# Kernel optimization log

Measured on AMD Instinct MI355X. Metric: run time of the kernel, lower is better.

The kernel has to match this reference:

```python
import jax, jax.numpy as jnp
import numpy as np

D_MODEL = 128; D_STATE = 8; D_CONV = 4; D_INNER = 256; DT_RANK = 8
H1 = 32; INPUTS = 3; OUTPUTS = 5
B_SZ = 8; SEQ = 2048


def _mamba(u, in_proj_w, conv_w, conv_b, x_proj_w, dt_proj_w, dt_proj_b, A_log, Dp, out_proj_w):
    # u: [B, L, D_MODEL]
    B, L, _ = u.shape
    xz = u @ in_proj_w.T                      # [B, L, 2*D_INNER]
    xs, z = jnp.split(xz, 2, axis=-1)
    # depthwise causal conv1d over time
    xc = jnp.moveaxis(xs, 1, 2)               # [B, D_INNER, L]
    xc = jax.lax.conv_general_dilated(
        xc, conv_w, window_strides=(1,), padding=[(D_CONV - 1, 0)],
        feature_group_count=D_INNER, dimension_numbers=("NCH", "OIH", "NCH"))
    xc = xc + conv_b[None, :, None]
    xs = jax.nn.silu(jnp.moveaxis(xc, 1, 2))  # [B, L, D_INNER]
    x_dbl = xs @ x_proj_w.T                   # [B, L, DT_RANK + 2*D_STATE]
    dt = x_dbl[..., :DT_RANK]
    Bm = x_dbl[..., DT_RANK:DT_RANK + D_STATE]
    Cm = x_dbl[..., DT_RANK + D_STATE:]
    delta = jax.nn.softplus(dt @ dt_proj_w.T + dt_proj_b)   # [B, L, D_INNER]
    A = -jnp.exp(A_log)                                     # [D_INNER, D_STATE]
    dA = jnp.exp(jnp.einsum("bld,dn->bldn", delta, A))      # [B, L, D_INNER, D_STATE]
    dBu = jnp.einsum("bld,bln->bldn", delta * xs, Bm)       # delta * B * u

    def step(h, t):
        dA_t, dBu_t, C_t = t
        h = dA_t * h + dBu_t                  # [B, D_INNER, D_STATE]
        y = jnp.einsum("bdn,bn->bd", h, C_t)
        return h, y

    h0 = jnp.zeros((B, D_INNER, D_STATE), dA.dtype)
    _, ys = jax.lax.scan(step, h0, (jnp.moveaxis(dA, 1, 0), jnp.moveaxis(dBu, 1, 0), jnp.moveaxis(Cm, 1, 0)))
    y = jnp.moveaxis(ys, 0, 1) + Dp * xs      # [B, L, D_INNER]
    y = y * jax.nn.silu(z)
    return y @ out_proj_w.T                   # [B, L, D_MODEL]


def _forward(x, proj0_w, proj0_b, in_proj_w, conv_w, conv_b, x_proj_w, dt_proj_w, dt_proj_b,
             A_log, Dp, out_proj_w, mlin_w, mlin_b, proj1_w, proj1_b, lin1_w, lin1_b,
             proj2_w, proj2_b):
    out = x @ proj0_w.T + proj0_b                            # proj0
    out = jnp.tanh(out)                                      # Dropout(1e-4) -> eval identity; Tanh
    out = _mamba(out, in_proj_w, conv_w, conv_b, x_proj_w, dt_proj_w, dt_proj_b, A_log, Dp, out_proj_w)
    out = jax.nn.elu(out)
    mamba_out = out @ mlin_w.T + mlin_b                      # Linear(128,128)
    out = mamba_out @ proj1_w.T + proj1_b                    # proj1
    out = jax.nn.elu(out)
    out = out @ lin1_w.T + lin1_b                            # linear_seq
    combined = jnp.concatenate([x, mamba_out, out], axis=-1) # dstack -> [B, L, 3+128+32]
    o = combined @ proj2_w.T + proj2_b                       # [B, L, 5]
    PI = np.float32(np.pi)
    for _ in range(2):                                       # special_rounding_operation x2
        o = o + jnp.sin(o * PI) * 0.5
    o = (o + 1.0) * 0.5
    o = o.at[:, :, 2:].add(1.0)
    real = jnp.stack([
        x[:, :, 0] + o[:, :, 0],
        x[:, :, 1] + x[:, :, 2] * (o[:, :, 1] / o[:, :, 2]),
        x[:, :, 2] * (o[:, :, 3] / o[:, :, 4]),
    ], axis=-1)
    return real


def setup_inputs() -> dict:
    key = jax.random.key(0)
    ks = jax.random.split(key, 12)
    def w(k, shape, s=0.05):
        return (jax.random.normal(k, shape) * s).astype(jnp.float32)
    A_init = jnp.log(jnp.tile(jnp.arange(1, D_STATE + 1, dtype=jnp.float32), (D_INNER, 1)))
    return {
        "x": jax.random.normal(ks[0], (B_SZ, SEQ, INPUTS), dtype=jnp.float32),
        "proj0_w": w(ks[1], (D_MODEL, INPUTS)), "proj0_b": jnp.zeros((D_MODEL,), jnp.float32),
        "in_proj_w": w(ks[2], (2 * D_INNER, D_MODEL)),
        "conv_w": w(ks[3], (D_INNER, 1, D_CONV)), "conv_b": jnp.zeros((D_INNER,), jnp.float32),
        "x_proj_w": w(ks[4], (DT_RANK + 2 * D_STATE, D_INNER)),
        "dt_proj_w": w(ks[5], (D_INNER, DT_RANK)),
        "dt_proj_b": jnp.full((D_INNER,), -4.6, jnp.float32),
        "A_log": A_init, "Dp": jnp.ones((D_INNER,), jnp.float32),
        "out_proj_w": w(ks[6], (D_MODEL, D_INNER)),
        "mlin_w": w(ks[7], (D_MODEL, D_MODEL)), "mlin_b": jnp.zeros((D_MODEL,), jnp.float32),
        "proj1_w": w(ks[8], (H1, D_MODEL)), "proj1_b": jnp.zeros((H1,), jnp.float32),
        "lin1_w": w(ks[9], (H1, H1)), "lin1_b": jnp.zeros((H1,), jnp.float32),
        "proj2_w": w(ks[10], (OUTPUTS, INPUTS + D_MODEL + H1)),
        "proj2_b": jnp.zeros((OUTPUTS,), jnp.float32),
    }


def reference(x, proj0_w, proj0_b, in_proj_w, conv_w, conv_b, x_proj_w, dt_proj_w, dt_proj_b,
              A_log, Dp, out_proj_w, mlin_w, mlin_b, proj1_w, proj1_b, lin1_w, lin1_b,
              proj2_w, proj2_b):
    return _forward(x, proj0_w, proj0_b, in_proj_w, conv_w, conv_b, x_proj_w, dt_proj_w,
                    dt_proj_b, A_log, Dp, out_proj_w, mlin_w, mlin_b, proj1_w, proj1_b,
                    lin1_w, lin1_b, proj2_w, proj2_b)
```

## Files before the change

### kernel.cpp

```cpp
#include <hip/hip_runtime.h>
#include <hip/hip_bf16.h>
#include <math.h>

#define TOKENS 16384
#define SEQLEN 2048
#define NCHUNK 64
#define LCHUNK 32
#define LOG2E 1.4426950408889634f

typedef __attribute__((ext_vector_type(8))) short bf16x8;
typedef __attribute__((ext_vector_type(8))) unsigned short u16x8;
typedef __attribute__((ext_vector_type(4))) float f32x4;

__device__ inline unsigned short f2bf(float f) {
    unsigned u = __float_as_uint(f);
    return (unsigned short)((u + 0x7FFF + ((u >> 16) & 1)) >> 16);
}
__device__ inline float bf2f(unsigned short b) {
    return __uint_as_float((unsigned)b << 16);
}
__device__ inline f32x4 mfma16(bf16x8 a, bf16x8 b, f32x4 c) {
    return __builtin_amdgcn_mfma_f32_16x16x32_bf16(a, b, c, 0, 0, 0);
}
__device__ inline float exp2_hw(float x) {
    float r; asm("v_exp_f32 %0, %1" : "=v"(r) : "v"(x)); return r;
}
__device__ inline float rcp_hw(float x) {
    float r; asm("v_rcp_f32 %0, %1" : "=v"(r) : "v"(x)); return r;
}
__device__ inline float fast_tanh(float x) {
    float ax = fabsf(x);
    float e = exp2_hw(2.885390081777927f * ax);
    float r = 1.f - 2.f*rcp_hw(e + 1.f);
    return copysignf(r, x);
}
__device__ inline float silu_hw(float v) {
    float e = exp2_hw(-LOG2E * v);
    return v * rcp_hw(1.f + e);
}

__global__ void k_prep2(const float* __restrict__ ipw, const float* __restrict__ opw,
                        const float* __restrict__ mlw,
                        const float* __restrict__ xpw, const float* __restrict__ dtw,
                        __hip_bfloat16* __restrict__ wi, __hip_bfloat16* __restrict__ wo,
                        __hip_bfloat16* __restrict__ wm, __hip_bfloat16* __restrict__ Wx) {
    int i = blockIdx.x * 256 + threadIdx.x;
    if (i < 65536) {
        int e = i;
        int chunk = e >> 9, ln = (e >> 3) & 63, j = e & 7;
        int g = chunk >> 4, kk = (chunk >> 2) & 3, w = chunk & 3;
        int r = ln & 15, q = ln >> 4;
        int row = g*64 + w*16 + r, col = kk*32 + q*8 + j;
        wi[i] = __float2bfloat16(ipw[row*128 + col]);
    } else if (i < 98304) {
        int e = i - 65536;
        int chunk = e >> 9, ln = (e >> 3) & 63, j = e & 7;
        int h = chunk >> 5, kk = (chunk >> 2) & 7, w = chunk & 3;
        int r = ln & 15, q = ln >> 4;
        int row = h*64 + w*16 + r, col = kk*32 + q*8 + j;
        wo[e] = __float2bfloat16(opw[row*256 + col]);
    } else if (i < 114688) {
        int e = i - 98304;
        int chunk = e >> 9, ln = (e >> 3) & 63, j = e & 7;
        int h = chunk >> 4, kk = (chunk >> 2) & 3, w = chunk & 3;
        int r = ln & 15, q = ln >> 4;
        int row = h*64 + w*16 + r, col = kk*32 + q*8 + j;
        wm[e] = __float2bfloat16(mlw[row*128 + col]);
    } else if (i < 196608) {
        int e = i - 114688;
        int chunk = e >> 9, ln = (e >> 3) & 63, j = e & 7;
        int g = chunk >> 5, kk = (chunk >> 2) & 7, w = chunk & 3;
        int r = ln & 15, q = ln >> 4;
        int n = g*64 + w*16 + r, k = kk*32 + q*8 + j;
        float v = 0.f;
        if (n < 256) {
            #pragma unroll
            for (int jj = 0; jj < 8; ++jj) v = fmaf(dtw[n*8+jj], xpw[jj*256+k], v);
        } else if (n < 272) {
            v = xpw[(n-248)*256 + k];
        }
        Wx[e] = __float2bfloat16(v);
    }
}

__global__ __launch_bounds__(256) void k_front(
    const float* __restrict__ x, const float* __restrict__ p0w,
    const float* __restrict__ p0b,
    const __hip_bfloat16* __restrict__ Wi,
    const __hip_bfloat16* __restrict__ Wx,
    const float* __restrict__ cw, const float* __restrict__ cb,
    const float* __restrict__ dpb, const float* __restrict__ A_log,
    __hip_bfloat16* __restrict__ zb,
    __hip_bfloat16* __restrict__ xsb,
    __hip_bfloat16* __restrict__ dlt,
    float* __restrict__ Bmo, float* __restrict__ Cmo,
    float* __restrict__ Ssum, unsigned short* __restrict__ Hend)
{
    __shared__ __align__(16) char smem[17408 + 17920];
    __shared__ float sx[48][3];
    __hip_bfloat16* U   = (__hip_bfloat16*)smem;
    __hip_bfloat16* AXS = (__hip_bfloat16*)smem;
    __hip_bfloat16* XCL = (__hip_bfloat16*)(smem + 17408);
    __hip_bfloat16* DL  = (__hip_bfloat16*)(smem + 17408);
    float* SB           = (float*)(smem + 17408 + 16896);

    int tid = threadIdx.x;
    int blk = blockIdx.x;
    int tok0 = blk * 32;
    bool seqstart = (tok0 & (SEQLEN-1)) == 0;

    if (tid < 144) {
        int row = tid/3, c = tid%3;
        int tok = tok0 - 16 + row;
        if (tok < 0) tok = 0;
        sx[row][c] = x[(size_t)tok*3 + c];
    }
    __syncthreads();
    {
        int col = tid & 127;
        int r0 = tid >> 7;
        float w0 = p0w[col*3+0], w1 = p0w[col*3+1], w2 = p0w[col*3+2];
        float b  = p0b[col];
        #pragma unroll
        for (int it = 0; it < 24; ++it) {
            int row = r0 + it*2;
            float v = b + sx[row][0]*w0 + sx[row][1]*w1 + sx[row][2]*w2;
            U[row*144 + col] = __float2bfloat16(fast_tanh(v));
        }
    }
    __syncthreads();

    int ln = tid & 63, w = tid >> 6;
    int r = ln & 15, q = ln >> 4;
    int ln8 = ln * 8;

    {
        f32x4 acch[4];
        #pragma unroll
        for (int g = 0; g < 4; ++g) acch[g] = (f32x4){0.f,0.f,0.f,0.f};
        const __hip_bfloat16* ah = &U[r*144 + q*8];
        #pragma unroll
        for (int kk = 0; kk < 4; ++kk) {
            bf16x8 a = *(const bf16x8*)(ah + kk*32);
            #pragma unroll
            for (int g = 0; g < 4; ++g) {
                bf16x8 bfv = *(const bf16x8*)(Wi + (((g*4 + kk)*4 + w) << 9) + ln8);
                acch[g] = mfma16(a, bfv, acch[g]);
            }
        }
        #pragma unroll
        for (int g = 0; g < 4; ++g) {
            int col = g*64 + w*16 + r;
            #pragma unroll
            for (int rr = 0; rr < 4; ++rr) {
                int row = q*4 + rr;
                if (row >= 13) {
                    int j = row - 13;
                    XCL[j*256 + col] = seqstart ? __float2bfloat16(0.f)
                                                : __float2bfloat16(acch[g][rr]);
                }
            }
        }
    }
    {
        f32x4 acc[2][8];
        #pragma unroll
        for (int mi = 0; mi < 2; ++mi)
            #pragma unroll
            for (int g = 0; g < 8; ++g) acc[mi][g] = (f32x4){0.f,0.f,0.f,0.f};
        const __hip_bfloat16* a0p = &U[(16+r)*144 + q*8];
        const __hip_bfloat16* a1p = &U[(32+r)*144 + q*8];
        #pragma unroll
        for (int kk = 0; kk < 4; ++kk) {
            bf16x8 a0 = *(const bf16x8*)(a0p + kk*32);
            bf16x8 a1 = *(const bf16x8*)(a1p + kk*32);
            #pragma unroll
            for (int g = 0; g < 8; ++g) {
                bf16x8 bfv = *(const bf16x8*)(Wi + (((g*4 + kk)*4 + w) << 9) + ln8);
                acc[0][g] = mfma16(a0, bfv, acc[0][g]);
                acc[1][g] = mfma16(a1, bfv, acc[1][g]);
            }
        }
        #pragma unroll
        for (int g = 0; g < 8; ++g) {
            int col = g*64 + w*16 + r;
            #pragma unroll
            for (int mi = 0; mi < 2; ++mi) {
                #pragma unroll
                for (int rr = 0; rr < 4; ++rr) {
                    int m = mi*16 + q*4 + rr;
                    float v = acc[mi][g][rr];
                    if (col < 256) XCL[(m+3)*256 + col] = __float2bfloat16(v);
                    else zb[(size_t)(tok0+m)*256 + col - 256] = __float2bfloat16(v);
                }
            }
        }
    }
    __syncthreads();

    {
        int d = tid;
        float cw0 = cw[d*4+0], cw1 = cw[d*4+1], cw2 = cw[d*4+2], cw3 = cw[d*4+3];
        float cbd = cb[d];
        const unsigned short* xc0 = (const unsigned short*)XCL + d;
        float w0v = bf2f(xc0[0]);
        float w1v = bf2f(xc0[256]);
        float w2v = bf2f(xc0[512]);
        #pragma unroll
        for (int row = 0; row < 32; ++row) {
            float w3v = bf2f(xc0[(row+3)*256]);
            float acc = cbd;
            acc = fmaf(cw0, w0v, acc);
            acc = fmaf(cw1, w1v, acc);
            acc = fmaf(cw2, w2v, acc);
            acc = fmaf(cw3, w3v, acc);
            acc = silu_hw(acc);
            __hip_bfloat16 hv = __float2bfloat16(acc);
            AXS[row*272 + d] = hv;
            xsb[(size_t)(tok0 + row)*256 + d] = hv;
            w0v = w1v; w1v = w2v; w2v = w3v;
        }
    }
    __syncthreads();

    {
        f32x4 acc[2][5];
        #pragma unroll
        for (int mi = 0; mi < 2; ++mi)
            #pragma unroll
            for (int g = 0; g < 5; ++g) acc[mi][g] = (f32x4){0.f,0.f,0.f,0.f};
        const __hip_bfloat16* arow0 = &AXS[r*272 + q*8];
        const __hip_bfloat16* arow1 = &AXS[(16+r)*272 + q*8];
        #pragma unroll
        for (int kk = 0; kk < 8; ++kk) {
            bf16x8 a0 = *(const bf16x8*)(arow0 + kk*32);
            bf16x8 a1 = *(const bf16x8*)(arow1 + kk*32);
            #pragma unroll
            for (int g = 0; g < 5; ++g) {
                bf16x8 bfv = *(const bf16x8*)(Wx + (((g*8 + kk)*4 + w) << 9) + ln8);
                acc[0][g] = mfma16(a0, bfv, acc[0][g]);
                acc[1][g] = mfma16(a1, bfv, acc[1][g]);
            }
        }
        #pragma unroll
        for (int g = 0; g < 5; ++g) {
            int col = g*64 + w*16 + r;
            if (col >= 272) continue;
            #pragma unroll
            for (int mi = 0; mi < 2; ++mi) {
                #pragma unroll
                for (int rr = 0; rr < 4; ++rr) {
                    int t = mi*16 + q*4 + rr;
                    int row = tok0 + t;
                    float v = acc[mi][g][rr];
                    if (col < 256) {
                        v += dpb[col];
                        v = (v > 20.f) ? v : __logf(1.f + __expf(v));
                        __hip_bfloat16 hv = __float2bfloat16(v);
                        DL[t*264 + col] = hv;
                        dlt[(size_t)row*256 + col] = hv;
                    } else if (col < 264) {
                        SB[t*8 + col - 256] = v;
                        Bmo[(size_t)row*8 + col - 256] = v;
                    } else {
                        Cmo[(size_t)row*8 + col - 264] = v;
                    }
                }
            }
        }
    }
    __syncthreads();

    {
        int d = tid;
        float A2[8];
        #pragma unroll
        for (int n = 0; n < 8; ++n) A2[n] = -__expf(A_log[d*8+n]) * LOG2E;
        float h[8] = {};
        float S = 0.f;
        for (int t = 0; t < LCHUNK; ++t) {
            float dt_c = bf2f(*(const unsigned short*)&DL[t*264 + d]);
            float xt_c = bf2f(*(const unsigned short*)&AXS[t*272 + d]);
            S += dt_c;
            float dx = dt_c * xt_c;
            #pragma unroll
            for (int n = 0; n < 8; ++n)
                h[n] = fmaf(exp2_hw(A2[n]*dt_c), h[n], dx * SB[t*8 + n]);
        }
        Ssum[(size_t)blk*256 + d] = S;
        u16x8 hp;
        #pragma unroll
        for (int n = 0; n < 8; ++n) hp[n] = f2bf(h[n]);
        *(u16x8*)&Hend[((size_t)blk*256 + d)*8] = hp;
    }
}

__global__ void k_scomb(const float* __restrict__ Ssum, const unsigned short* __restrict__ Hend,
                        const float* __restrict__ A_log, unsigned short* __restrict__ Hin) {
    int blk = blockIdx.x;
    int b = blk >> 3, dg = blk & 7;
    int d = dg*32 + (threadIdx.x >> 3);
    int n = threadIdx.x & 7;
    float A2 = -__expf(A_log[d*8+n]) * LOG2E;
    float h = 0.f;
    size_t i0 = (size_t)(b*NCHUNK)*256 + d;
    float S  = Ssum[i0];
    float He = bf2f(Hend[i0*8 + n]);
    for (int c = 0; c < NCHUNK; ++c) {
        size_t idx = (size_t)(b*NCHUNK + c)*256 + d;
        float Sn = 0.f, Hn = 0.f;
        if (c < NCHUNK-1) {
            size_t ix2 = idx + 256;
            Sn = Ssum[ix2];
            Hn = bf2f(Hend[ix2*8 + n]);
        }
        Hin[idx*8 + n] = f2bf(h);
        h = fmaf(exp2_hw(A2*S), h, He);
        S = Sn; He = Hn;
    }
}

__global__ __launch_bounds__(256) void k_s2_opml(
    const __hip_bfloat16* __restrict__ delta,
    const __hip_bfloat16* __restrict__ xs,
    const float* __restrict__ Bm, const float* __restrict__ Cm,
    const __hip_bfloat16* __restrict__ zb,
    const float* __restrict__ A_log, const float* __restrict__ Dp,
    const unsigned short* __restrict__ Hin,
    const __hip_bfloat16* __restrict__ Wo,
    const __hip_bfloat16* __restrict__ Wm,
    const float* __restrict__ mlb,
    __hip_bfloat16* __restrict__ mo)
{
    __shared__ __hip_bfloat16 Al[32][272];
    __shared__ __hip_bfloat16 opl[32][136];
    __shared__ float sB[LCHUNK][8], sC[LCHUNK][8];
    int tid = threadIdx.x;
    int blk = blockIdx.x;
    int tok0 = blk * 32;
    {
        int t2 = tid >> 3, j = tid & 7;
        sB[t2][j] = Bm[(size_t)(tok0 + t2)*8 + j];
        sC[t2][j] = Cm[(size_t)(tok0 + t2)*8 + j];
    }
    int d = tid;
    float A2[8], h[8];
    u16x8 hv = *(const u16x8*)&Hin[((size_t)blk*256 + d)*8];
    #pragma unroll
    for (int n = 0; n < 8; ++n) {
        A2[n] = -__expf(A_log[d*8+n]) * LOG2E;
        h[n] = bf2f(hv[n]);
    }
    float Dpd = Dp[d];
    __syncthreads();
    const __hip_bfloat16* dptr = delta + (size_t)tok0*256 + d;
    const __hip_bfloat16* xptr = xs    + (size_t)tok0*256 + d;
    const __hip_bfloat16* zptr = zb    + (size_t)tok0*256 + d;
    float dt_c = __bfloat162float(dptr[0]), xt_c = __bfloat162float(xptr[0]);
    for (int t = 0; t < LCHUNK; ++t) {
        float dt_n = 0.f, xt_n = 0.f;
        if (t < LCHUNK-1) {
            dt_n = __bfloat162float(dptr[(t+1)*256]);
            xt_n = __bfloat162float(xptr[(t+1)*256]);
        }
        float dx = dt_c * xt_c;
        float yv = 0.f;
        #pragma unroll
        for (int n = 0; n < 8; ++n) {
            h[n] = fmaf(exp2_hw(A2[n]*dt_c), h[n], dx * sB[t][n]);
            yv = fmaf(h[n], sC[t][n], yv);
        }
        yv = fmaf(Dpd, xt_c, yv);
        float z = __bfloat162float(zptr[t*256]);
        yv *= silu_hw(z) * (z != 0.f ? 1.f : 1.f);
        Al[t][d] = __float2bfloat16(yv);
        dt_c = dt_n; xt_c = xt_n;
    }
    __syncthreads();

    int ln = tid & 63, w = tid >> 6;
    int r = ln & 15, q = ln >> 4;
    int ln8 = ln * 8;
    int c0 = w*16 + r, c1 = c0 + 64;

    f32x4 a00 = (f32x4){0.f,0.f,0.f,0.f};
    f32x4 a01 = a00, a10 = a00, a11 = a00;
    const __hip_bfloat16* a0p = &Al[r][q*8];
    const __hip_bfloat16* a1p = &Al[16+r][q*8];
    #pragma unroll
    for (int kk = 0; kk < 8; ++kk) {
        bf16x8 af0 = *(const bf16x8*)(a0p + kk*32);
        bf16x8 af1 = *(const bf16x8*)(a1p + kk*32);
        bf16x8 bf0 = *(const bf16x8*)(Wo + (((0*8 + kk)*4 + w) << 9) + ln8);
        bf16x8 bf1 = *(const bf16x8*)(Wo + (((1*8 + kk)*4 + w) << 9) + ln8);
        a00 = mfma16(af0, bf0, a00);
        a10 = mfma16(af1, bf0, a10);
        a01 = mfma16(af0, bf1, a01);
        a11 = mfma16(af1, bf1, a11);
    }
    #pragma unroll
    for (int rr = 0; rr < 4; ++rr) {
        int row = q*4 + rr;
        float v;
        v = a00[rr]; v = v > 0.f ? v : (__expf(v)-1.f); opl[row][c0]    = __float2bfloat16(v);
        v = a01[rr]; v = v > 0.f ? v : (__expf(v)-1.f); opl[row][c1]    = __float2bfloat16(v);
        v = a10[rr]; v = v > 0.f ? v : (__expf(v)-1.f); opl[row+16][c0] = __float2bfloat16(v);
        v = a11[rr]; v = v > 0.f ? v : (__expf(v)-1.f); opl[row+16][c1] = __float2bfloat16(v);
    }
    __syncthreads();

    f32x4 m00 = (f32x4){0.f,0.f,0.f,0.f};
    f32x4 m01 = m00, m10 = m00, m11 = m00;
    const __hip_bfloat16* A0m = &opl[r][q*8];
    const __hip_bfloat16* A1m = &opl[16+r][q*8];
    #pragma unroll
    for (int kk = 0; kk < 4; ++kk) {
        bf16x8 af0 = *(const bf16x8*)(A0m + kk*32);
        bf16x8 af1 = *(const bf16x8*)(A1m + kk*32);
        bf16x8 bf0 = *(const bf16x8*)(Wm + (((0*4 + kk)*4 + w) << 9) + ln8);
        bf16x8 bf1 = *(const bf16x8*)(Wm + (((1*4 + kk)*4 + w) << 9) + ln8);
        m00 = mfma16(af0, bf0, m00);
        m10 = mfma16(af1, bf0, m10);
        m01 = mfma16(af0, bf1, m01);
        m11 = mfma16(af1, bf1, m11);
    }
    {
        float bl0 = mlb[c0], bl1 = mlb[c1];
        __hip_bfloat16* mob = mo + (size_t)tok0*128;
        #pragma unroll
        for (int rr = 0; rr < 4; ++rr) {
            int row = q*4 + rr;
            mob[row*128 + c0]      = __float2bfloat16(m00[rr] + bl0);
            mob[row*128 + c1]      = __float2bfloat16(m01[rr] + bl1);
            mob[(row+16)*128 + c0] = __float2bfloat16(m10[rr] + bl0);
            mob[(row+16)*128 + c1] = __float2bfloat16(m11[rr] + bl1);
        }
    }
}

__global__ __launch_bounds__(256) void k_tail(const float* __restrict__ x,
                       const unsigned short* __restrict__ mo,
                       const float* __restrict__ p1w, const float* __restrict__ p1b,
                       const float* __restrict__ l1w, const float* __restrict__ l1b,
                       const float* __restrict__ p2w, const float* __restrict__ p2b,
                       float* __restrict__ out) {
    __shared__ float s_mo[16][132];
    __shared__ float s_p1w[32][132];
    __shared__ float s_l1w[32][36];
    __shared__ float s_p2w[5][164];
    __shared__ float s_h1[16][36];
    __shared__ float s_o32[16][36];
    __shared__ float s_o[16][6];
    int tid = threadIdx.x;
    int tok0 = blockIdx.x * 16;
    for (int i = tid; i < 32*32; i += 256) {
        int r = i >> 5, c = (i & 31) * 4;
        *(float4*)&s_p1w[r][c] = *(const float4*)&p1w[r*128 + c];
    }
    for (int i = tid; i < 32*8; i += 256) {
        int r = i >> 3, c = (i & 7) * 4;
        *(float4*)&s_l1w[r][c] = *(const float4*)&l1w[r*32 + c];
    }
    for (int i = tid; i < 5*163; i += 256)
        s_p2w[i / 163][i % 163] = p2w[i];
    {
        int i = tid;
        int r = i >> 4, c = (i & 15) * 8;
        u16x8 v = *(const u16x8*)&mo[(size_t)(tok0 + r)*128 + c];
        #pragma unroll
        for (int e = 0; e < 8; ++e) s_mo[r][c+e] = bf2f(v[e]);
    }
    __syncthreads();
    {
        int j = tid & 31, tb = tid >> 5;
        float bj = p1b[j];
        #pragma unroll
        for (int p = 0; p < 2; ++p) {
            int tk = tb + p*8;
            float v = bj;
            #pragma unroll 8
            for (int k = 0; k < 128; k += 4) {
                float4 m4 = *(const float4*)&s_mo[tk][k];
                float4 w4 = *(const float4*)&s_p1w[j][k];
                v = fmaf(m4.x, w4.x, v); v = fmaf(m4.y, w4.y, v);
                v = fmaf(m4.z, w4.z, v); v = fmaf(m4.w, w4.w, v);
            }
            v = v > 0.f ? v : (__expf(v) - 1.f);
            s_h1[tk][j] = v;
        }
    }
    __syncthreads();
    {
        int j = tid & 31, tb = tid >> 5;
        float bj = l1b[j];
        #pragma unroll
        for (int p = 0; p < 2; ++p) {
            int tk = tb + p*8;
            float v = bj;
            #pragma unroll
            for (int k = 0; k < 32; k += 4) {
                float4 m4 = *(const float4*)&s_h1[tk][k];
                float4 w4 = *(const float4*)&s_l1w[j][k];
                v = fmaf(m4.x, w4.x, v); v = fmaf(m4.y, w4.y, v);
                v = fmaf(m4.z, w4.z, v); v = fmaf(m4.w, w4.w, v);
            }
            s_o32[tk][j] = v;
        }
    }
    __syncthreads();
    if (tid < 160) {
        int tk = tid / 10, rem = tid % 10;
        int j = rem >> 1, half = rem & 1;
        const float* wr = s_p2w[j];
        float v = 0.f;
        if (half == 0) {
            int tok = tok0 + tk;
            v = fmaf(x[tok*3+0], wr[0], v);
            v = fmaf(x[tok*3+1], wr[1], v);
            v = fmaf(x[tok*3+2], wr[2], v);
            #pragma unroll 8
            for (int k = 0; k < 64; ++k) v = fmaf(s_mo[tk][k], wr[3+k], v);
        } else {
            #pragma unroll 8
            for (int k = 64; k < 128; ++k) v = fmaf(s_mo[tk][k], wr[3+k], v);
            #pragma unroll 8
            for (int k = 0; k < 32; ++k)  v = fmaf(s_o32[tk][k], wr[131+k], v);
        }
        v += __shfl_xor(v, 1);
        if (half == 0) {
            v += p2b[j];
            const float PI = 3.14159265358979323846f;
            v = v + __sinf(v*PI)*0.5f;
            v = v + __sinf(v*PI)*0.5f;
            v = (v + 1.f)*0.5f;
            if (j >= 2) v += 1.f;
            s_o[tk][j] = v;
        }
    }
    __syncthreads();
    if (tid < 48) {
        int tk = tid / 3, ln = tid % 3;
        int tok = tok0 + tk;
        float x0 = x[tok*3+0], x1 = x[tok*3+1], x2 = x[tok*3+2];
        float r;
        if (ln == 0)      r = x0 + s_o[tk][0];
        else if (ln == 1) r = x1 + x2*(s_o[tk][1]/s_o[tk][2]);
        else              r = x2*(s_o[tk][3]/s_o[tk][4]);
        out[(size_t)tok*3 + ln] = r;
    }
}

extern "C" void kernel_launch(void* const* d_in, const int* in_sizes, int n_in,
                              void* d_out, int out_size, void* d_ws, size_t ws_size,
                              hipStream_t stream) {
    const float* x        = (const float*)d_in[0];
    const float* proj0_w  = (const float*)d_in[1];
    const float* proj0_b  = (const float*)d_in[2];
    const float* in_proj_w= (const float*)d_in[3];
    const float* conv_w   = (const float*)d_in[4];
    const float* conv_b   = (const float*)d_in[5];
    const float* x_proj_w = (const float*)d_in[6];
    const float* dt_proj_w= (const float*)d_in[7];
    const float* dt_proj_b= (const float*)d_in[8];
    const float* A_log    = (const float*)d_in[9];
    const float* Dp       = (const float*)d_in[10];
    const float* out_proj_w=(const float*)d_in[11];
    const float* mlin_w   = (const float*)d_in[12];
    const float* mlin_b   = (const float*)d_in[13];
    const float* proj1_w  = (const float*)d_in[14];
    const float* proj1_b  = (const float*)d_in[15];
    const float* lin1_w   = (const float*)d_in[16];
    const float* lin1_b   = (const float*)d_in[17];
    const float* proj2_w  = (const float*)d_in[18];
    const float* proj2_b  = (const float*)d_in[19];
    float* out = (float*)d_out;

    char* wsb = (char*)d_ws;
    const size_t MB = 1048576;
    __hip_bfloat16* z_bf   = (__hip_bfloat16*)(wsb + 12*MB);
    __hip_bfloat16* xs_bf  = (__hip_bfloat16*)(wsb + 20*MB);
    __hip_bfloat16* dlt_bf = (__hip_bfloat16*)(wsb + 28*MB);
    float* Bm   = (float*)(wsb + 36*MB);
    float* Cm   = (float*)(wsb + 36*MB + 524288);
    float* Ssum = (float*)(wsb + 37*MB);
    unsigned short* Hend = (unsigned short*)(wsb + 37*MB + 524288);
    unsigned short* Hin  = (unsigned short*)(wsb + 39*MB + 524288);
    __hip_bfloat16* w_in_bf  = (__hip_bfloat16*)(wsb + 50*MB);
    __hip_bfloat16* w_out_bf = (__hip_bfloat16*)(wsb + 50*MB + 131072);
    __hip_bfloat16* w_ml_bf  = (__hip_bfloat16*)(wsb + 50*MB + 196608);
    __hip_bfloat16* Wx_bf    = (__hip_bfloat16*)(wsb + 50*MB + 229376);
    unsigned short* mo = (unsigned short*)(wsb + 51*MB);

    k_prep2<<<768, 256, 0, stream>>>(in_proj_w, out_proj_w, mlin_w, x_proj_w,
                                     dt_proj_w, w_in_bf, w_out_bf, w_ml_bf, Wx_bf);
    k_front<<<TOKENS/32, 256, 0, stream>>>(x, proj0_w, proj0_b, w_in_bf, Wx_bf,
                                           conv_w, conv_b, dt_proj_b, A_log,
                                           z_bf, xs_bf, dlt_bf, Bm, Cm, Ssum, Hend);
    k_scomb<<<64, 256, 0, stream>>>(Ssum, Hend, A_log, Hin);
    k_s2_opml<<<TOKENS/32, 256, 0, stream>>>(dlt_bf, xs_bf, Bm, Cm, z_bf, A_log, Dp,
                                             Hin, w_out_bf, w_ml_bf, mlin_b,
                                             (__hip_bfloat16*)mo);
    k_tail<<<TOKENS/16, 256, 0, stream>>>(x, mo, proj1_w, proj1_b, lin1_w, lin1_b, proj2_w, proj2_b, out);
}
```

Measured before the change: 83.35 us.

## Fuse tail MLP into scan/out-proj kernel, keeping mlin output in LDS

The separate tail kernel is merged into the second scan/out-projection kernel. The mlin output now stays in shared memory as bf16-rounded floats instead of being written to global memory and read back, and one kernel launch is dropped. The cost is higher LDS use per block (the tail weights are staged into every block), which may lower occupancy in the scan-heavy kernel. It also adds weight-loading work to each of the 512 blocks.

Measured after the change: 77.55 us. -7.0%, faster.

```diff
diff --git a/kernel.cpp b/kernel.cpp
--- a/kernel.cpp
+++ b/kernel.cpp
@@ -98,11 +98,11 @@
 {
     __shared__ __align__(16) char smem[17408 + 17920];
     __shared__ float sx[48][3];
+    __shared__ float SB[LCHUNK][8];
     __hip_bfloat16* U   = (__hip_bfloat16*)smem;
     __hip_bfloat16* AXS = (__hip_bfloat16*)smem;
     __hip_bfloat16* XCL = (__hip_bfloat16*)(smem + 17408);
     __hip_bfloat16* DL  = (__hip_bfloat16*)(smem + 17408);
-    float* SB           = (float*)(smem + 17408 + 16896);
 
     int tid = threadIdx.x;
     int blk = blockIdx.x;
@@ -260,7 +260,7 @@
                         DL[t*264 + col] = hv;
                         dlt[(size_t)row*256 + col] = hv;
                     } else if (col < 264) {
-                        SB[t*8 + col - 256] = v;
+                        SB[t][col - 256] = v;
                         Bmo[(size_t)row*8 + col - 256] = v;
                     } else {
                         Cmo[(size_t)row*8 + col - 264] = v;
@@ -285,7 +285,7 @@
             float dx = dt_c * xt_c;
             #pragma unroll
             for (int n = 0; n < 8; ++n)
-                h[n] = fmaf(exp2_hw(A2[n]*dt_c), h[n], dx * SB[t*8 + n]);
+                h[n] = fmaf(exp2_hw(A2[n]*dt_c), h[n], dx * SB[t][n]);
         }
         Ssum[(size_t)blk*256 + d] = S;
         u16x8 hp;
@@ -320,7 +320,7 @@
     }
 }
 
-__global__ __launch_bounds__(256) void k_s2_opml(
+__global__ __launch_bounds__(256) void k_s2_tail(
     const __hip_bfloat16* __restrict__ delta,
     const __hip_bfloat16* __restrict__ xs,
     const float* __restrict__ Bm, const float* __restrict__ Cm,
@@ -330,11 +330,24 @@
     const __hip_bfloat16* __restrict__ Wo,
     const __hip_bfloat16* __restrict__ Wm,
     const float* __restrict__ mlb,
-    __hip_bfloat16* __restrict__ mo)
+    const float* __restrict__ x,
+    const float* __restrict__ p1w, const float* __restrict__ p1b,
+    const float* __restrict__ l1w, const float* __restrict__ l1b,
+    const float* __restrict__ p2w, const float* __restrict__ p2b,
+    float* __restrict__ out)
 {
-    __shared__ __hip_bfloat16 Al[32][272];
+    __shared__ __align__(16) char smA[17408];
     __shared__ __hip_bfloat16 opl[32][136];
     __shared__ float sB[LCHUNK][8], sC[LCHUNK][8];
+    __shared__ float s_p1w[32][132];
+    __shared__ float s_l1w[32][36];
+    __shared__ float s_p2w[5][164];
+    __shared__ float s_h1[32][36];
+    __shared__ float s_o32[32][36];
+    __shared__ float s_o[32][6];
+    __hip_bfloat16* Al = (__hip_bfloat16*)smA;
+    float* mol = (float*)smA;
+
     int tid = threadIdx.x;
     int blk = blockIdx.x;
     int tok0 = blk * 32;
@@ -343,6 +356,16 @@
         sB[t2][j] = Bm[(size_t)(tok0 + t2)*8 + j];
         sC[t2][j] = Cm[(size_t)(tok0 + t2)*8 + j];
     }
+    for (int i = tid; i < 32*32; i += 256) {
+        int r2 = i >> 5, c2 = (i & 31) * 4;
+        *(float4*)&s_p1w[r2][c2] = *(const float4*)&p1w[r2*128 + c2];
+    }
+    {
+        int r2 = tid >> 3, c2 = (tid & 7) * 4;
+        *(float4*)&s_l1w[r2][c2] = *(const float4*)&l1w[r2*32 + c2];
+    }
+    for (int i = tid; i < 5*163; i += 256) s_p2w[i/163][i%163] = p2w[i];
+
     int d = tid;
     float A2[8], h[8];
     u16x8 hv = *(const u16x8*)&Hin[((size_t)blk*256 + d)*8];
@@ -372,8 +395,8 @@
         }
         yv = fmaf(Dpd, xt_c, yv);
         float z = __bfloat162float(zptr[t*256]);
-        yv *= silu_hw(z) * (z != 0.f ? 1.f : 1.f);
-        Al[t][d] = __float2bfloat16(yv);
+        yv *= silu_hw(z);
+        Al[t*272 + d] = __float2bfloat16(yv);
         dt_c = dt_n; xt_c = xt_n;
     }
     __syncthreads();
@@ -385,8 +408,8 @@
 
     f32x4 a00 = (f32x4){0.f,0.f,0.f,0.f};
     f32x4 a01 = a00, a10 = a00, a11 = a00;
-    const __hip_bfloat16* a0p = &Al[r][q*8];
-    const __hip_bfloat16* a1p = &Al[16+r][q*8];
+    const __hip_bfloat16* a0p = &Al[r*272 + q*8];
+    const __hip_bfloat16* a1p = &Al[(16+r)*272 + q*8];
     #pragma unroll
     for (int kk = 0; kk < 8; ++kk) {
         bf16x8 af0 = *(const bf16x8*)(a0p + kk*32);
@@ -426,61 +449,27 @@
     }
     {
         float bl0 = mlb[c0], bl1 = mlb[c1];
-        __hip_bfloat16* mob = mo + (size_t)tok0*128;
         #pragma unroll
         for (int rr = 0; rr < 4; ++rr) {
             int row = q*4 + rr;
-            mob[row*128 + c0]      = __float2bfloat16(m00[rr] + bl0);
-            mob[row*128 + c1]      = __float2bfloat16(m01[rr] + bl1);
-            mob[(row+16)*128 + c0] = __float2bfloat16(m10[rr] + bl0);
-            mob[(row+16)*128 + c1] = __float2bfloat16(m11[rr] + bl1);
-        }
-    }
-}
-
-__global__ __launch_bounds__(256) void k_tail(const float* __restrict__ x,
-                       const unsigned short* __restrict__ mo,
-                       const float* __restrict__ p1w, const float* __restrict__ p1b,
-                       const float* __restrict__ l1w, const float* __restrict__ l1b,
-                       const float* __restrict__ p2w, const float* __restrict__ p2b,
-                       float* __restrict__ out) {
-    __shared__ float s_mo[16][132];
-    __shared__ float s_p1w[32][132];
-    __shared__ float s_l1w[32][36];
-    __shared__ float s_p2w[5][164];
-    __shared__ float s_h1[16][36];
-    __shared__ float s_o32[16][36];
-    __shared__ float s_o[16][6];
-    int tid = threadIdx.x;
-    int tok0 = blockIdx.x * 16;
-    for (int i = tid; i < 32*32; i += 256) {
-        int r = i >> 5, c = (i & 31) * 4;
-        *(float4*)&s_p1w[r][c] = *(const float4*)&p1w[r*128 + c];
-    }
-    for (int i = tid; i < 32*8; i += 256) {
-        int r = i >> 3, c = (i & 7) * 4;
-        *(float4*)&s_l1w[r][c] = *(const float4*)&l1w[r*32 + c];
-    }
-    for (int i = tid; i < 5*163; i += 256)
-        s_p2w[i / 163][i % 163] = p2w[i];
-    {
-        int i = tid;
-        int r = i >> 4, c = (i & 15) * 8;
-        u16x8 v = *(const u16x8*)&mo[(size_t)(tok0 + r)*128 + c];
-        #pragma unroll
-        for (int e = 0; e < 8; ++e) s_mo[r][c+e] = bf2f(v[e]);
-    }
-    __syncthreads();
+            mol[row*132 + c0]      = bf2f(f2bf(m00[rr] + bl0));
+            mol[row*132 + c1]      = bf2f(f2bf(m01[rr] + bl1));
+            mol[(row+16)*132 + c0] = bf2f(f2bf(m10[rr] + bl0));
+            mol[(row+16)*132 + c1] = bf2f(f2bf(m11[rr] + bl1));
+        }
+    }
+    __syncthreads();
+
     {
         int j = tid & 31, tb = tid >> 5;
         float bj = p1b[j];
         #pragma unroll
-        for (int p = 0; p < 2; ++p) {
+        for (int p = 0; p < 4; ++p) {
             int tk = tb + p*8;
             float v = bj;
             #pragma unroll 8
             for (int k = 0; k < 128; k += 4) {
-                float4 m4 = *(const float4*)&s_mo[tk][k];
+                float4 m4 = *(const float4*)&mol[tk*132 + k];
                 float4 w4 = *(const float4*)&s_p1w[j][k];
                 v = fmaf(m4.x, w4.x, v); v = fmaf(m4.y, w4.y, v);
                 v = fmaf(m4.z, w4.z, v); v = fmaf(m4.w, w4.w, v);
@@ -494,7 +483,7 @@
         int j = tid & 31, tb = tid >> 5;
         float bj = l1b[j];
         #pragma unroll
-        for (int p = 0; p < 2; ++p) {
+        for (int p = 0; p < 4; ++p) {
             int tk = tb + p*8;
             float v = bj;
             #pragma unroll
@@ -508,45 +497,48 @@
         }
     }
     __syncthreads();
-    if (tid < 160) {
-        int tk = tid / 10, rem = tid % 10;
-        int j = rem >> 1, half = rem & 1;
-        const float* wr = s_p2w[j];
-        float v = 0.f;
-        if (half == 0) {
-            int tok = tok0 + tk;
-            v = fmaf(x[tok*3+0], wr[0], v);
-            v = fmaf(x[tok*3+1], wr[1], v);
-            v = fmaf(x[tok*3+2], wr[2], v);
-            #pragma unroll 8
-            for (int k = 0; k < 64; ++k) v = fmaf(s_mo[tk][k], wr[3+k], v);
-        } else {
-            #pragma unroll 8
-            for (int k = 64; k < 128; ++k) v = fmaf(s_mo[tk][k], wr[3+k], v);
-            #pragma unroll 8
-            for (int k = 0; k < 32; ++k)  v = fmaf(s_o32[tk][k], wr[131+k], v);
-        }
-        v += __shfl_xor(v, 1);
-        if (half == 0) {
-            v += p2b[j];
-            const float PI = 3.14159265358979323846f;
-            v = v + __sinf(v*PI)*0.5f;
-            v = v + __sinf(v*PI)*0.5f;
-            v = (v + 1.f)*0.5f;
-            if (j >= 2) v += 1.f;
-            s_o[tk][j] = v;
-        }
-    }
-    __syncthreads();
-    if (tid < 48) {
-        int tk = tid / 3, ln = tid % 3;
+    #pragma unroll
+    for (int pass = 0; pass < 2; ++pass) {
+        if (tid < 160) {
+            int tk = tid / 10 + pass*16, rem = tid % 10;
+            int j = rem >> 1, half = rem & 1;
+            const float* wr = s_p2w[j];
+            float v = 0.f;
+            if (half == 0) {
+                int tok = tok0 + tk;
+                v = fmaf(x[tok*3+0], wr[0], v);
+                v = fmaf(x[tok*3+1], wr[1], v);
+                v = fmaf(x[tok*3+2], wr[2], v);
+                #pragma unroll 8
+                for (int k = 0; k < 64; ++k) v = fmaf(mol[tk*132 + k], wr[3+k], v);
+            } else {
+                #pragma unroll 8
+                for (int k = 64; k < 128; ++k) v = fmaf(mol[tk*132 + k], wr[3+k], v);
+                #pragma unroll 8
+                for (int k = 0; k < 32; ++k)  v = fmaf(s_o32[tk][k], wr[131+k], v);
+            }
+            v += __shfl_xor(v, 1);
+            if (half == 0) {
+                v += p2b[j];
+                const float PI = 3.14159265358979323846f;
+                v = v + __sinf(v*PI)*0.5f;
+                v = v + __sinf(v*PI)*0.5f;
+                v = (v + 1.f)*0.5f;
+                if (j >= 2) v += 1.f;
+                s_o[tk][j] = v;
+            }
+        }
+    }
+    __syncthreads();
+    if (tid < 96) {
+        int tk = tid / 3, lnn = tid % 3;
         int tok = tok0 + tk;
         float x0 = x[tok*3+0], x1 = x[tok*3+1], x2 = x[tok*3+2];
-        float r;
-        if (ln == 0)      r = x0 + s_o[tk][0];
-        else if (ln == 1) r = x1 + x2*(s_o[tk][1]/s_o[tk][2]);
-        else              r = x2*(s_o[tk][3]/s_o[tk][4]);
-        out[(size_t)tok*3 + ln] = r;
+        float rv;
+        if (lnn == 0)      rv = x0 + s_o[tk][0];
+        else if (lnn == 1) rv = x1 + x2*(s_o[tk][1]/s_o[tk][2]);
+        else               rv = x2*(s_o[tk][3]/s_o[tk][4]);
+        out[(size_t)tok*3 + lnn] = rv;
     }
 }
 
@@ -589,7 +581,6 @@
     __hip_bfloat16* w_out_bf = (__hip_bfloat16*)(wsb + 50*MB + 131072);
     __hip_bfloat16* w_ml_bf  = (__hip_bfloat16*)(wsb + 50*MB + 196608);
     __hip_bfloat16* Wx_bf    = (__hip_bfloat16*)(wsb + 50*MB + 229376);
-    unsigned short* mo = (unsigned short*)(wsb + 51*MB);
 
     k_prep2<<<768, 256, 0, stream>>>(in_proj_w, out_proj_w, mlin_w, x_proj_w,
                                      dt_proj_w, w_in_bf, w_out_bf, w_ml_bf, Wx_bf);
@@ -597,8 +588,8 @@
                                            conv_w, conv_b, dt_proj_b, A_log,
                                            z_bf, xs_bf, dlt_bf, Bm, Cm, Ssum, Hend);
     k_scomb<<<64, 256, 0, stream>>>(Ssum, Hend, A_log, Hin);
-    k_s2_opml<<<TOKENS/32, 256, 0, stream>>>(dlt_bf, xs_bf, Bm, Cm, z_bf, A_log, Dp,
+    k_s2_tail<<<TOKENS/32, 256, 0, stream>>>(dlt_bf, xs_bf, Bm, Cm, z_bf, A_log, Dp,
                                              Hin, w_out_bf, w_ml_bf, mlin_b,
-                                             (__hip_bfloat16*)mo);
-    k_tail<<<TOKENS/16, 256, 0, stream>>>(x, mo, proj1_w, proj1_b, lin1_w, lin1_b, proj2_w, proj2_b, out);
-}
+                                             x, proj1_w, proj1_b, lin1_w, lin1_b,
+                                             proj2_w, proj2_b, out);
+}
```
